# Kernel optimization log

Hardware: AMD Instinct MI355X
Metric: run time of the kernel (lower is better)

Reference implementation:

```python
import jax, jax.numpy as jnp
import numpy as np
from functools import partial

NUM_CLASSES = 6
IMG_H, IMG_W = 512, 512


def rasterize_boxes(bboxes, num_classes, hw):
    # bboxes: [B, num_organs, 4] int (xmin, ymin, xmax, ymax)
    H, W = hw
    bb = bboxes.astype(jnp.int32)
    xmin = jnp.clip(bb[..., 0], 0, W - 1)
    ymin = jnp.clip(bb[..., 1], 0, H - 1)
    xmax = jnp.maximum(xmin, jnp.minimum(bb[..., 2], W))
    ymax = jnp.maximum(ymin, jnp.minimum(bb[..., 3], H))
    rows = jnp.arange(H)[None, None, :, None]   # [1,1,H,1]
    cols = jnp.arange(W)[None, None, None, :]   # [1,1,1,W]
    mask = ((rows >= ymin[..., None, None]) & (rows < ymax[..., None, None]) &
            (cols >= xmin[..., None, None]) & (cols < xmax[..., None, None]))
    organs = mask.astype(jnp.float32)           # [B, num_organs, H, W]
    B = bboxes.shape[0]
    bg = jnp.zeros((B, 1, H, W), jnp.float32)   # channel 0 (background) stays 0
    return jnp.concatenate([bg, organs], axis=1)  # [B, num_classes, H, W]


def conv2d(x, w, stride=1, pad=0):
    return jax.lax.conv_general_dilated(
        x, w, window_strides=(stride, stride),
        padding=[(pad, pad), (pad, pad)],
        dimension_numbers=('NCHW', 'OIHW', 'NCHW'))


def bilinear_align_corners(x, out_h, out_w):
    # F.interpolate(..., mode='bilinear', align_corners=True)
    B, C, H, W = x.shape
    ys = jnp.linspace(0.0, H - 1.0, out_h)
    xs = jnp.linspace(0.0, W - 1.0, out_w)
    y0 = jnp.floor(ys).astype(jnp.int32); y1 = jnp.minimum(y0 + 1, H - 1)
    x0 = jnp.floor(xs).astype(jnp.int32); x1 = jnp.minimum(x0 + 1, W - 1)
    wy = (ys - y0).astype(x.dtype)[:, None]     # [out_h,1]
    wx = (xs - x0).astype(x.dtype)              # [out_w]
    top = x[:, :, y0, :]                        # [B,C,out_h,W]
    bot = x[:, :, y1, :]
    row = top * (1 - wy) + bot * wy             # [B,C,out_h,W]
    return row[..., x0] * (1 - wx) + row[..., x1] * wx


def sag(X_dec_c, X_dec_k, W_alpha, W_expand):
    attended = X_dec_c * X_dec_k
    alpha = jax.nn.softmax(conv2d(attended, W_alpha), axis=1)  # [B,num_classes,h,w]
    alpha_exp = conv2d(alpha, W_expand)                         # [B,C_sem,h,w]
    gated = jax.nn.sigmoid(X_dec_c * alpha_exp)
    return X_dec_c + gated


def setup_inputs() -> dict:
    key = jax.random.key(0)
    ks = jax.random.split(key, 6)
    B, C_sem, h, w = 4, 512, 32, 32
    num_organs = NUM_CLASSES - 1
    enc_final = jax.random.normal(ks[0], (B, C_sem, h, w), jnp.float32)
    bboxes = jax.random.randint(ks[1], (B, num_organs, 4), 0, IMG_W, jnp.int32)
    W_proc = jax.random.normal(ks[2], (C_sem, NUM_CLASSES, 3, 3), jnp.float32) * 0.1
    b_proc = jax.random.normal(ks[3], (C_sem,), jnp.float32) * 0.1
    W_alpha = jax.random.normal(ks[4], (NUM_CLASSES, C_sem, 1, 1), jnp.float32) * 0.05
    W_expand = jax.random.normal(ks[5], (C_sem, NUM_CLASSES, 1, 1), jnp.float32) * 0.05
    return {"enc_final": enc_final, "bboxes": bboxes, "W_proc": W_proc,
            "b_proc": b_proc, "W_alpha": W_alpha, "W_expand": W_expand}


def reference(enc_final, bboxes, W_proc, b_proc, W_alpha, W_expand):
    one_hot_map = rasterize_boxes(bboxes, NUM_CLASSES, (IMG_H, IMG_W))
    # Conv2d(num_classes -> enc_final_channels, k=3, s=2, p=1) + ReLU
    proc = jax.nn.relu(conv2d(one_hot_map, W_proc, stride=2, pad=1)
                       + b_proc[None, :, None, None])
    X_dec_k = bilinear_align_corners(proc, enc_final.shape[2], enc_final.shape[3])
    sag_out = sag(enc_final, X_dec_k, W_alpha, W_expand)
    return sag_out, one_hot_map, X_dec_k
```

## Files before the change

### kernel.cpp

```cpp
#include <hip/hip_runtime.h>
#include <math.h>

#define BATCH 4
#define CSEM 512
#define NORG 5
#define NCLS 6
#define HIMG 512
#define WIMG 512
#define HS 32
#define PH 256

#define SAG_N (BATCH*CSEM*HS*HS)
#define OH_N  (BATCH*NCLS*HIMG*WIMG)
#define OH_OFF SAG_N
#define XK_OFF (SAG_N + OH_N)

__global__ void k_raster(const int* __restrict__ bb, float* __restrict__ oh) {
    int idx = blockIdx.x * blockDim.x + threadIdx.x;
    int x4 = (idx & 127) << 2;
    int t  = idx >> 7;
    int y  = t & 511;
    int bc = t >> 9;
    int ch = bc % NCLS;
    int b  = bc / NCLS;
    float4 v = make_float4(0.f, 0.f, 0.f, 0.f);
    if (ch != 0) {
        const int* p = bb + (b * NORG + (ch - 1)) * 4;
        int xmin = min(max(p[0], 0), WIMG - 1);
        int ymin = min(max(p[1], 0), HIMG - 1);
        int xmax = max(xmin, min(p[2], WIMG));
        int ymax = max(ymin, min(p[3], HIMG));
        if (y >= ymin && y < ymax) {
            v.x = (x4 + 0 >= xmin && x4 + 0 < xmax) ? 1.f : 0.f;
            v.y = (x4 + 1 >= xmin && x4 + 1 < xmax) ? 1.f : 0.f;
            v.z = (x4 + 2 >= xmin && x4 + 2 < xmax) ? 1.f : 0.f;
            v.w = (x4 + 3 >= xmin && x4 + 3 < xmax) ? 1.f : 0.f;
        }
    }
    reinterpret_cast<float4*>(oh)[idx] = v;
}

__global__ void k_xdeck(const int* __restrict__ bb, const float* __restrict__ Wp,
                        const float* __restrict__ bp, float* __restrict__ xk) {
    int blk = blockIdx.x;
    int cg = blk & 7;
    int oy = (blk >> 3) & 31;
    int b  = blk >> 8;
    int t  = threadIdx.x;
    int x  = t & 31;
    int c0 = t >> 5;

    float ysf = (float)(oy * 255.0 / 31.0);
    int y0 = (int)floorf(ysf);
    int y1 = min(y0 + 1, PH - 1);
    float wy = ysf - (float)y0;
    float xsf = (float)(x * 255.0 / 31.0);
    int x0 = (int)floorf(xsf);
    int x1 = min(x0 + 1, PH - 1);
    float wx = xsf - (float)x0;

    float ry0f[NORG][3], ry1f[NORG][3], cx0f[NORG][3], cx1f[NORG][3];
    bool act[NORG];
#pragma unroll
    for (int i = 0; i < NORG; i++) {
        const int* p = bb + (b * NORG + i) * 4;
        int xmin = min(max(p[0], 0), WIMG - 1);
        int ymin = min(max(p[1], 0), HIMG - 1);
        int xmax = max(xmin, min(p[2], WIMG));
        int ymax = max(ymin, min(p[3], HIMG));
        bool anyr = false, anyc = false;
#pragma unroll
        for (int k = 0; k < 3; k++) {
            int r0 = 2 * y0 - 1 + k, r1 = 2 * y1 - 1 + k;
            int cA = 2 * x0 - 1 + k, cB = 2 * x1 - 1 + k;
            float f0 = (r0 >= ymin && r0 < ymax) ? 1.f : 0.f;
            float f1 = (r1 >= ymin && r1 < ymax) ? 1.f : 0.f;
            float g0 = (cA >= xmin && cA < xmax) ? 1.f : 0.f;
            float g1 = (cB >= xmin && cB < xmax) ? 1.f : 0.f;
            ry0f[i][k] = f0; ry1f[i][k] = f1; cx0f[i][k] = g0; cx1f[i][k] = g1;
            anyr = anyr || (f0 > 0.f) || (f1 > 0.f);
            anyc = anyc || (g0 > 0.f) || (g1 > 0.f);
        }
        act[i] = anyr && anyc;
    }

    int cbase = cg * 64 + c0 * 8;
    float P[8][4];
#pragma unroll
    for (int cc = 0; cc < 8; cc++) {
        float bv = bp[cbase + cc];
        P[cc][0] = bv; P[cc][1] = bv; P[cc][2] = bv; P[cc][3] = bv;
    }

#pragma unroll
    for (int i = 0; i < NORG; i++) {
        if (!act[i]) continue;
        float c00 = cx0f[i][0], c01 = cx0f[i][1], c02 = cx0f[i][2];
        float c10 = cx1f[i][0], c11 = cx1f[i][1], c12 = cx1f[i][2];
        float r00 = ry0f[i][0], r01 = ry0f[i][1], r02 = ry0f[i][2];
        float r10 = ry1f[i][0], r11 = ry1f[i][1], r12 = ry1f[i][2];
#pragma unroll
        for (int cc = 0; cc < 8; cc++) {
            const float* w = Wp + (size_t)((cbase + cc) * NCLS + i + 1) * 9;
            float w0 = w[0], w1 = w[1], w2 = w[2];
            float w3 = w[3], w4 = w[4], w5 = w[5];
            float w6 = w[6], w7 = w[7], w8 = w[8];
            float s00 = w0 * c00 + w1 * c01 + w2 * c02;
            float s01 = w3 * c00 + w4 * c01 + w5 * c02;
            float s02 = w6 * c00 + w7 * c01 + w8 * c02;
            float s10 = w0 * c10 + w1 * c11 + w2 * c12;
            float s11 = w3 * c10 + w4 * c11 + w5 * c12;
            float s12 = w6 * c10 + w7 * c11 + w8 * c12;
            P[cc][0] += s00 * r00 + s01 * r01 + s02 * r02;
            P[cc][1] += s10 * r00 + s11 * r01 + s12 * r02;
            P[cc][2] += s00 * r10 + s01 * r11 + s02 * r12;
            P[cc][3] += s10 * r10 + s11 * r11 + s12 * r12;
        }
    }

#pragma unroll
    for (int cc = 0; cc < 8; cc++) {
        int c = cbase + cc;
        float p00 = fmaxf(P[cc][0], 0.f);
        float p01 = fmaxf(P[cc][1], 0.f);
        float p10 = fmaxf(P[cc][2], 0.f);
        float p11 = fmaxf(P[cc][3], 0.f);
        float t0 = p00 * (1.f - wy) + p10 * wy;
        float t1 = p01 * (1.f - wy) + p11 * wy;
        float val = t0 * (1.f - wx) + t1 * wx;
        xk[((b * CSEM + c) * HS + oy) * HS + x] = val;
    }
}

__global__ void k_logits(const float* __restrict__ enc, const float* __restrict__ xk,
                         const float* __restrict__ Wa, float* __restrict__ part) {
    int blk = blockIdx.x;
    int cg = blk & 3;
    int oy = (blk >> 2) & 31;
    int b  = blk >> 7;
    int t  = threadIdx.x;
    int x  = t & 31;
    int c0 = t >> 5;
    float acc[NCLS] = {0, 0, 0, 0, 0, 0};
    for (int k = 0; k < 16; k++) {
        int c = cg * 128 + k * 8 + c0;
        int idx = ((b * CSEM + c) * HS + oy) * HS + x;
        float att = enc[idx] * xk[idx];
#pragma unroll
        for (int o = 0; o < NCLS; o++) acc[o] += Wa[o * CSEM + c] * att;
    }
    __shared__ float red[NCLS][8][32];
#pragma unroll
    for (int o = 0; o < NCLS; o++) red[o][c0][x] = acc[o];
    __syncthreads();
    if (t < NCLS * 32) {
        int o = t >> 5;
        int xx = t & 31;
        float s = 0.f;
#pragma unroll
        for (int j = 0; j < 8; j++) s += red[o][j][xx];
        part[(((cg * BATCH + b) * NCLS + o) * HS + oy) * HS + xx] = s;
    }
}

__global__ void k_softmax(const float* __restrict__ part, float* __restrict__ alpha) {
    int idx = blockIdx.x * blockDim.x + threadIdx.x;
    if (idx >= BATCH * HS * HS) return;
    int x = idx & 31, oy = (idx >> 5) & 31, b = idx >> 10;
    float l[NCLS];
#pragma unroll
    for (int o = 0; o < NCLS; o++) {
        float s = 0.f;
#pragma unroll
        for (int cg = 0; cg < 4; cg++)
            s += part[(((cg * BATCH + b) * NCLS + o) * HS + oy) * HS + x];
        l[o] = s;
    }
    float m = l[0];
#pragma unroll
    for (int o = 1; o < NCLS; o++) m = fmaxf(m, l[o]);
    float sum = 0.f;
#pragma unroll
    for (int o = 0; o < NCLS; o++) { l[o] = expf(l[o] - m); sum += l[o]; }
    float inv = 1.f / sum;
#pragma unroll
    for (int o = 0; o < NCLS; o++)
        alpha[((b * NCLS + o) * HS + oy) * HS + x] = l[o] * inv;
}

__global__ void k_sag(const float* __restrict__ enc, const float* __restrict__ We,
                      const float* __restrict__ alpha, float* __restrict__ out) {
    int idx = blockIdx.x * blockDim.x + threadIdx.x;
    int x4 = (idx & 7) << 2;
    int oy = (idx >> 3) & 31;
    int c  = (idx >> 8) & 511;
    int b  = idx >> 17;
    float4 e = reinterpret_cast<const float4*>(enc)[idx];
    float4 ae = make_float4(0.f, 0.f, 0.f, 0.f);
#pragma unroll
    for (int o = 0; o < NCLS; o++) {
        float w = We[c * NCLS + o];
        const float4 a = *reinterpret_cast<const float4*>(
            alpha + ((b * NCLS + o) * HS + oy) * HS + x4);
        ae.x += w * a.x; ae.y += w * a.y; ae.z += w * a.z; ae.w += w * a.w;
    }
    float4 r;
    r.x = e.x + 1.f / (1.f + expf(-e.x * ae.x));
    r.y = e.y + 1.f / (1.f + expf(-e.y * ae.y));
    r.z = e.z + 1.f / (1.f + expf(-e.z * ae.z));
    r.w = e.w + 1.f / (1.f + expf(-e.w * ae.w));
    reinterpret_cast<float4*>(out)[idx] = r;
}

extern "C" void kernel_launch(void* const* d_in, const int* in_sizes, int n_in,
                              void* d_out, int out_size, void* d_ws, size_t ws_size,
                              hipStream_t stream) {
    const float* enc = (const float*)d_in[0];
    const int*   bb  = (const int*)d_in[1];
    const float* Wp  = (const float*)d_in[2];
    const float* bp  = (const float*)d_in[3];
    const float* Wa  = (const float*)d_in[4];
    const float* We  = (const float*)d_in[5];
    float* out = (float*)d_out;
    float* sag = out;
    float* oh  = out + OH_OFF;
    float* xk  = out + XK_OFF;
    float* part  = oh;
    float* alpha = oh + 98304;

    k_xdeck  <<<BATCH * 32 * 8, 256, 0, stream>>>(bb, Wp, bp, xk);
    k_logits <<<BATCH * 32 * 4, 256, 0, stream>>>(enc, xk, Wa, part);
    k_softmax<<<16, 256, 0, stream>>>(part, alpha);
    k_sag    <<<SAG_N / 4 / 256, 256, 0, stream>>>(enc, We, alpha, sag);
    k_raster <<<OH_N / 4 / 256, 256, 0, stream>>>(bb, oh);
}
```

Before: 97.89 us.

## Fuse xdeck with logits and softmax with sag into two kernels

Computes attention logits directly inside the X_dec_k kernel from register values, which removes the xk re-read and one launch. Softmax is recomputed per block in shared memory and fused into the SAG gating kernel, so the alpha buffer and the softmax launch go away. This cuts five launches to three and reduces global traffic, at the cost of redundant softmax work in each block and fewer, larger-work blocks for the SAG stage (512 blocks).

```diff
diff --git a/kernel.cpp b/kernel.cpp
--- a/kernel.cpp
+++ b/kernel.cpp
@@ -14,6 +14,178 @@
 #define OH_N  (BATCH*NCLS*HIMG*WIMG)
 #define OH_OFF SAG_N
 #define XK_OFF (SAG_N + OH_N)
+
+__global__ void k_xdeck_logits(const int* __restrict__ bb, const float* __restrict__ Wp,
+                               const float* __restrict__ bp, const float* __restrict__ enc,
+                               const float* __restrict__ Wa, float* __restrict__ xk,
+                               float* __restrict__ part) {
+    int blk = blockIdx.x;
+    int cg = blk & 7;
+    int oy = (blk >> 3) & 31;
+    int b  = blk >> 8;
+    int t  = threadIdx.x;
+    int x  = t & 31;
+    int c0 = t >> 5;
+
+    float ysf = (float)(oy * 255.0 / 31.0);
+    int y0 = (int)floorf(ysf);
+    int y1 = min(y0 + 1, PH - 1);
+    float wy = ysf - (float)y0;
+    float xsf = (float)(x * 255.0 / 31.0);
+    int x0 = (int)floorf(xsf);
+    int x1 = min(x0 + 1, PH - 1);
+    float wx = xsf - (float)x0;
+
+    float ry0f[NORG][3], ry1f[NORG][3], cx0f[NORG][3], cx1f[NORG][3];
+    bool act[NORG];
+#pragma unroll
+    for (int i = 0; i < NORG; i++) {
+        const int* p = bb + (b * NORG + i) * 4;
+        int xmin = min(max(p[0], 0), WIMG - 1);
+        int ymin = min(max(p[1], 0), HIMG - 1);
+        int xmax = max(xmin, min(p[2], WIMG));
+        int ymax = max(ymin, min(p[3], HIMG));
+        bool anyr = false, anyc = false;
+#pragma unroll
+        for (int k = 0; k < 3; k++) {
+            int r0 = 2 * y0 - 1 + k, r1 = 2 * y1 - 1 + k;
+            int cA = 2 * x0 - 1 + k, cB = 2 * x1 - 1 + k;
+            float f0 = (r0 >= ymin && r0 < ymax) ? 1.f : 0.f;
+            float f1 = (r1 >= ymin && r1 < ymax) ? 1.f : 0.f;
+            float g0 = (cA >= xmin && cA < xmax) ? 1.f : 0.f;
+            float g1 = (cB >= xmin && cB < xmax) ? 1.f : 0.f;
+            ry0f[i][k] = f0; ry1f[i][k] = f1; cx0f[i][k] = g0; cx1f[i][k] = g1;
+            anyr = anyr || (f0 > 0.f) || (f1 > 0.f);
+            anyc = anyc || (g0 > 0.f) || (g1 > 0.f);
+        }
+        act[i] = anyr && anyc;
+    }
+
+    int cbase = cg * 64 + c0 * 8;
+    float P[8][4];
+#pragma unroll
+    for (int cc = 0; cc < 8; cc++) {
+        float bv = bp[cbase + cc];
+        P[cc][0] = bv; P[cc][1] = bv; P[cc][2] = bv; P[cc][3] = bv;
+    }
+
+#pragma unroll
+    for (int i = 0; i < NORG; i++) {
+        if (!act[i]) continue;
+        float c00 = cx0f[i][0], c01 = cx0f[i][1], c02 = cx0f[i][2];
+        float c10 = cx1f[i][0], c11 = cx1f[i][1], c12 = cx1f[i][2];
+        float r00 = ry0f[i][0], r01 = ry0f[i][1], r02 = ry0f[i][2];
+        float r10 = ry1f[i][0], r11 = ry1f[i][1], r12 = ry1f[i][2];
+#pragma unroll
+        for (int cc = 0; cc < 8; cc++) {
+            const float* w = Wp + (size_t)((cbase + cc) * NCLS + i + 1) * 9;
+            float w0 = w[0], w1 = w[1], w2 = w[2];
+            float w3 = w[3], w4 = w[4], w5 = w[5];
+            float w6 = w[6], w7 = w[7], w8 = w[8];
+            float s00 = w0 * c00 + w1 * c01 + w2 * c02;
+            float s01 = w3 * c00 + w4 * c01 + w5 * c02;
+            float s02 = w6 * c00 + w7 * c01 + w8 * c02;
+            float s10 = w0 * c10 + w1 * c11 + w2 * c12;
+            float s11 = w3 * c10 + w4 * c11 + w5 * c12;
+            float s12 = w6 * c10 + w7 * c11 + w8 * c12;
+            P[cc][0] += s00 * r00 + s01 * r01 + s02 * r02;
+            P[cc][1] += s10 * r00 + s11 * r01 + s12 * r02;
+            P[cc][2] += s00 * r10 + s01 * r11 + s02 * r12;
+            P[cc][3] += s10 * r10 + s11 * r11 + s12 * r12;
+        }
+    }
+
+    float acc[NCLS] = {0, 0, 0, 0, 0, 0};
+#pragma unroll
+    for (int cc = 0; cc < 8; cc++) {
+        int c = cbase + cc;
+        float p00 = fmaxf(P[cc][0], 0.f);
+        float p01 = fmaxf(P[cc][1], 0.f);
+        float p10 = fmaxf(P[cc][2], 0.f);
+        float p11 = fmaxf(P[cc][3], 0.f);
+        float t0 = p00 * (1.f - wy) + p10 * wy;
+        float t1 = p01 * (1.f - wy) + p11 * wy;
+        float val = t0 * (1.f - wx) + t1 * wx;
+        int idx = ((b * CSEM + c) * HS + oy) * HS + x;
+        xk[idx] = val;
+        float att = enc[idx] * val;
+#pragma unroll
+        for (int o = 0; o < NCLS; o++) acc[o] += Wa[o * CSEM + c] * att;
+    }
+
+    __shared__ float red[NCLS][8][32];
+#pragma unroll
+    for (int o = 0; o < NCLS; o++) red[o][c0][x] = acc[o];
+    __syncthreads();
+    if (t < NCLS * 32) {
+        int o = t >> 5;
+        int xx = t & 31;
+        float s = 0.f;
+#pragma unroll
+        for (int j = 0; j < 8; j++) s += red[o][j][xx];
+        part[(((cg * BATCH + b) * NCLS + o) * HS + oy) * HS + xx] = s;
+    }
+}
+
+__global__ void k_softmax_sag(const float* __restrict__ part, const float* __restrict__ enc,
+                              const float* __restrict__ We, float* __restrict__ out) {
+    int blk = blockIdx.x;
+    int sl = blk & 3;
+    int oy = (blk >> 2) & 31;
+    int b  = blk >> 7;
+    int t  = threadIdx.x;
+
+    __shared__ float lg[NCLS][32];
+    if (t < NCLS * 32) {
+        int o = t >> 5;
+        int x = t & 31;
+        float s = 0.f;
+#pragma unroll
+        for (int cg = 0; cg < 8; cg++)
+            s += part[(((cg * BATCH + b) * NCLS + o) * HS + oy) * HS + x];
+        lg[o][x] = s;
+    }
+    __syncthreads();
+    if (t < 32) {
+        float l[NCLS];
+#pragma unroll
+        for (int o = 0; o < NCLS; o++) l[o] = lg[o][t];
+        float m = l[0];
+#pragma unroll
+        for (int o = 1; o < NCLS; o++) m = fmaxf(m, l[o]);
+        float sum = 0.f;
+#pragma unroll
+        for (int o = 0; o < NCLS; o++) { l[o] = expf(l[o] - m); sum += l[o]; }
+        float inv = 1.f / sum;
+#pragma unroll
+        for (int o = 0; o < NCLS; o++) lg[o][t] = l[o] * inv;
+    }
+    __syncthreads();
+
+    int x4 = (t & 7) << 2;
+    int cq = t >> 3;
+#pragma unroll
+    for (int j = 0; j < 4; j++) {
+        int c = sl * 128 + cq * 4 + j;
+        int idx4 = (((b * CSEM + c) * HS + oy) * HS + x4) >> 2;
+        float4 e = reinterpret_cast<const float4*>(enc)[idx4];
+        float4 ae = make_float4(0.f, 0.f, 0.f, 0.f);
+#pragma unroll
+        for (int o = 0; o < NCLS; o++) {
+            float w = We[c * NCLS + o];
+            ae.x += w * lg[o][x4 + 0];
+            ae.y += w * lg[o][x4 + 1];
+            ae.z += w * lg[o][x4 + 2];
+            ae.w += w * lg[o][x4 + 3];
+        }
+        float4 r;
+        r.x = e.x + 1.f / (1.f + expf(-e.x * ae.x));
+        r.y = e.y + 1.f / (1.f + expf(-e.y * ae.y));
+        r.z = e.z + 1.f / (1.f + expf(-e.z * ae.z));
+        r.w = e.w + 1.f / (1.f + expf(-e.w * ae.w));
+        reinterpret_cast<float4*>(out)[idx4] = r;
+    }
+}
 
 __global__ void k_raster(const int* __restrict__ bb, float* __restrict__ oh) {
     int idx = blockIdx.x * blockDim.x + threadIdx.x;
@@ -40,178 +212,6 @@
     reinterpret_cast<float4*>(oh)[idx] = v;
 }
 
-__global__ void k_xdeck(const int* __restrict__ bb, const float* __restrict__ Wp,
-                        const float* __restrict__ bp, float* __restrict__ xk) {
-    int blk = blockIdx.x;
-    int cg = blk & 7;
-    int oy = (blk >> 3) & 31;
-    int b  = blk >> 8;
-    int t  = threadIdx.x;
-    int x  = t & 31;
-    int c0 = t >> 5;
-
-    float ysf = (float)(oy * 255.0 / 31.0);
-    int y0 = (int)floorf(ysf);
-    int y1 = min(y0 + 1, PH - 1);
-    float wy = ysf - (float)y0;
-    float xsf = (float)(x * 255.0 / 31.0);
-    int x0 = (int)floorf(xsf);
-    int x1 = min(x0 + 1, PH - 1);
-    float wx = xsf - (float)x0;
-
-    float ry0f[NORG][3], ry1f[NORG][3], cx0f[NORG][3], cx1f[NORG][3];
-    bool act[NORG];
-#pragma unroll
-    for (int i = 0; i < NORG; i++) {
-        const int* p = bb + (b * NORG + i) * 4;
-        int xmin = min(max(p[0], 0), WIMG - 1);
-        int ymin = min(max(p[1], 0), HIMG - 1);
-        int xmax = max(xmin, min(p[2], WIMG));
-        int ymax = max(ymin, min(p[3], HIMG));
-        bool anyr = false, anyc = false;
-#pragma unroll
-        for (int k = 0; k < 3; k++) {
-            int r0 = 2 * y0 - 1 + k, r1 = 2 * y1 - 1 + k;
-            int cA = 2 * x0 - 1 + k, cB = 2 * x1 - 1 + k;
-            float f0 = (r0 >= ymin && r0 < ymax) ? 1.f : 0.f;
-            float f1 = (r1 >= ymin && r1 < ymax) ? 1.f : 0.f;
-            float g0 = (cA >= xmin && cA < xmax) ? 1.f : 0.f;
-            float g1 = (cB >= xmin && cB < xmax) ? 1.f : 0.f;
-            ry0f[i][k] = f0; ry1f[i][k] = f1; cx0f[i][k] = g0; cx1f[i][k] = g1;
-            anyr = anyr || (f0 > 0.f) || (f1 > 0.f);
-            anyc = anyc || (g0 > 0.f) || (g1 > 0.f);
-        }
-        act[i] = anyr && anyc;
-    }
-
-    int cbase = cg * 64 + c0 * 8;
-    float P[8][4];
-#pragma unroll
-    for (int cc = 0; cc < 8; cc++) {
-        float bv = bp[cbase + cc];
-        P[cc][0] = bv; P[cc][1] = bv; P[cc][2] = bv; P[cc][3] = bv;
-    }
-
-#pragma unroll
-    for (int i = 0; i < NORG; i++) {
-        if (!act[i]) continue;
-        float c00 = cx0f[i][0], c01 = cx0f[i][1], c02 = cx0f[i][2];
-        float c10 = cx1f[i][0], c11 = cx1f[i][1], c12 = cx1f[i][2];
-        float r00 = ry0f[i][0], r01 = ry0f[i][1], r02 = ry0f[i][2];
-        float r10 = ry1f[i][0], r11 = ry1f[i][1], r12 = ry1f[i][2];
-#pragma unroll
-        for (int cc = 0; cc < 8; cc++) {
-            const float* w = Wp + (size_t)((cbase + cc) * NCLS + i + 1) * 9;
-            float w0 = w[0], w1 = w[1], w2 = w[2];
-            float w3 = w[3], w4 = w[4], w5 = w[5];
-            float w6 = w[6], w7 = w[7], w8 = w[8];
-            float s00 = w0 * c00 + w1 * c01 + w2 * c02;
-            float s01 = w3 * c00 + w4 * c01 + w5 * c02;
-            float s02 = w6 * c00 + w7 * c01 + w8 * c02;
-            float s10 = w0 * c10 + w1 * c11 + w2 * c12;
-            float s11 = w3 * c10 + w4 * c11 + w5 * c12;
-            float s12 = w6 * c10 + w7 * c11 + w8 * c12;
-            P[cc][0] += s00 * r00 + s01 * r01 + s02 * r02;
-            P[cc][1] += s10 * r00 + s11 * r01 + s12 * r02;
-            P[cc][2] += s00 * r10 + s01 * r11 + s02 * r12;
-            P[cc][3] += s10 * r10 + s11 * r11 + s12 * r12;
-        }
-    }
-
-#pragma unroll
-    for (int cc = 0; cc < 8; cc++) {
-        int c = cbase + cc;
-        float p00 = fmaxf(P[cc][0], 0.f);
-        float p01 = fmaxf(P[cc][1], 0.f);
-        float p10 = fmaxf(P[cc][2], 0.f);
-        float p11 = fmaxf(P[cc][3], 0.f);
-        float t0 = p00 * (1.f - wy) + p10 * wy;
-        float t1 = p01 * (1.f - wy) + p11 * wy;
-        float val = t0 * (1.f - wx) + t1 * wx;
-        xk[((b * CSEM + c) * HS + oy) * HS + x] = val;
-    }
-}
-
-__global__ void k_logits(const float* __restrict__ enc, const float* __restrict__ xk,
-                         const float* __restrict__ Wa, float* __restrict__ part) {
-    int blk = blockIdx.x;
-    int cg = blk & 3;
-    int oy = (blk >> 2) & 31;
-    int b  = blk >> 7;
-    int t  = threadIdx.x;
-    int x  = t & 31;
-    int c0 = t >> 5;
-    float acc[NCLS] = {0, 0, 0, 0, 0, 0};
-    for (int k = 0; k < 16; k++) {
-        int c = cg * 128 + k * 8 + c0;
-        int idx = ((b * CSEM + c) * HS + oy) * HS + x;
-        float att = enc[idx] * xk[idx];
-#pragma unroll
-        for (int o = 0; o < NCLS; o++) acc[o] += Wa[o * CSEM + c] * att;
-    }
-    __shared__ float red[NCLS][8][32];
-#pragma unroll
-    for (int o = 0; o < NCLS; o++) red[o][c0][x] = acc[o];
-    __syncthreads();
-    if (t < NCLS * 32) {
-        int o = t >> 5;
-        int xx = t & 31;
-        float s = 0.f;
-#pragma unroll
-        for (int j = 0; j < 8; j++) s += red[o][j][xx];
-        part[(((cg * BATCH + b) * NCLS + o) * HS + oy) * HS + xx] = s;
-    }
-}
-
-__global__ void k_softmax(const float* __restrict__ part, float* __restrict__ alpha) {
-    int idx = blockIdx.x * blockDim.x + threadIdx.x;
-    if (idx >= BATCH * HS * HS) return;
-    int x = idx & 31, oy = (idx >> 5) & 31, b = idx >> 10;
-    float l[NCLS];
-#pragma unroll
-    for (int o = 0; o < NCLS; o++) {
-        float s = 0.f;
-#pragma unroll
-        for (int cg = 0; cg < 4; cg++)
-            s += part[(((cg * BATCH + b) * NCLS + o) * HS + oy) * HS + x];
-        l[o] = s;
-    }
-    float m = l[0];
-#pragma unroll
-    for (int o = 1; o < NCLS; o++) m = fmaxf(m, l[o]);
-    float sum = 0.f;
-#pragma unroll
-    for (int o = 0; o < NCLS; o++) { l[o] = expf(l[o] - m); sum += l[o]; }
-    float inv = 1.f / sum;
-#pragma unroll
-    for (int o = 0; o < NCLS; o++)
-        alpha[((b * NCLS + o) * HS + oy) * HS + x] = l[o] * inv;
-}
-
-__global__ void k_sag(const float* __restrict__ enc, const float* __restrict__ We,
-                      const float* __restrict__ alpha, float* __restrict__ out) {
-    int idx = blockIdx.x * blockDim.x + threadIdx.x;
-    int x4 = (idx & 7) << 2;
-    int oy = (idx >> 3) & 31;
-    int c  = (idx >> 8) & 511;
-    int b  = idx >> 17;
-    float4 e = reinterpret_cast<const float4*>(enc)[idx];
-    float4 ae = make_float4(0.f, 0.f, 0.f, 0.f);
-#pragma unroll
-    for (int o = 0; o < NCLS; o++) {
-        float w = We[c * NCLS + o];
-        const float4 a = *reinterpret_cast<const float4*>(
-            alpha + ((b * NCLS + o) * HS + oy) * HS + x4);
-        ae.x += w * a.x; ae.y += w * a.y; ae.z += w * a.z; ae.w += w * a.w;
-    }
-    float4 r;
-    r.x = e.x + 1.f / (1.f + expf(-e.x * ae.x));
-    r.y = e.y + 1.f / (1.f + expf(-e.y * ae.y));
-    r.z = e.z + 1.f / (1.f + expf(-e.z * ae.z));
-    r.w = e.w + 1.f / (1.f + expf(-e.w * ae.w));
-    reinterpret_cast<float4*>(out)[idx] = r;
-}
-
 extern "C" void kernel_launch(void* const* d_in, const int* in_sizes, int n_in,
                               void* d_out, int out_size, void* d_ws, size_t ws_size,
                               hipStream_t stream) {
@@ -225,12 +225,9 @@
     float* sag = out;
     float* oh  = out + OH_OFF;
     float* xk  = out + XK_OFF;
-    float* part  = oh;
-    float* alpha = oh + 98304;
-
-    k_xdeck  <<<BATCH * 32 * 8, 256, 0, stream>>>(bb, Wp, bp, xk);
-    k_logits <<<BATCH * 32 * 4, 256, 0, stream>>>(enc, xk, Wa, part);
-    k_softmax<<<16, 256, 0, stream>>>(part, alpha);
-    k_sag    <<<SAG_N / 4 / 256, 256, 0, stream>>>(enc, We, alpha, sag);
-    k_raster <<<OH_N / 4 / 256, 256, 0, stream>>>(bb, oh);
-}
+    float* part = oh;
+
+    k_xdeck_logits<<<BATCH * 32 * 8, 256, 0, stream>>>(bb, Wp, bp, enc, Wa, xk, part);
+    k_softmax_sag <<<BATCH * 32 * 4, 256, 0, stream>>>(part, enc, We, sag);
+    k_raster      <<<OH_N / 4 / 256, 256, 0, stream>>>(bb, oh);
+}
```

New measurement: 94.68 us. 3.3% less time.
